# Performance work log

Measured on AMD Instinct MI355X. Metric: run time of the kernel, lower is better.

Reference implementation:

```python
import jax, jax.numpy as jnp
import numpy as np

N_HEADS = 8
EPS = 1e-12  # F.normalize eps


def setup_inputs() -> dict:
    key = jax.random.key(0)
    ks = jax.random.split(key, 7)
    B, M, S, D = 2, 4, 2048, 512
    scale = 1.0 / np.sqrt(D)
    return {
        "x": jax.random.normal(ks[0], (B, M, S, D), dtype=jnp.float32),
        "Wq": jax.random.normal(ks[1], (D, D), dtype=jnp.float32) * scale,
        "bq": jax.random.normal(ks[2], (D,), dtype=jnp.float32) * 0.01,
        "Wkv": jax.random.normal(ks[3], (D, D), dtype=jnp.float32) * scale,
        "bkv": jax.random.normal(ks[4], (D,), dtype=jnp.float32) * 0.01,
        "Wo": jax.random.normal(ks[5], (D, D), dtype=jnp.float32) * scale,
        "bo": jax.random.normal(ks[6], (D,), dtype=jnp.float32) * 0.01,
    }


def _heads(t, H):
    # [B,M,S,D] -> [B,M,H,S,dk]
    B, Mo, S, D = t.shape
    return t.reshape(B, Mo, S, H, D // H).swapaxes(2, 3)


def reference(x, Wq, bq, Wkv, bkv, Wo, bo):
    B, Mo, S, D = x.shape
    H = N_HEADS
    # nn.Linear: y = x @ W^T + b
    Q = x @ Wq.T + bq
    KV = x @ Wkv.T + bkv  # K and V share this projection
    Qh = _heads(Q, H)
    Kh = _heads(KV, H)
    Vh = Kh
    # L2-normalize along head dim (cosine attention)
    Qn = Qh / jnp.maximum(jnp.linalg.norm(Qh, axis=-1, keepdims=True), EPS)
    Kn = Kh / jnp.maximum(jnp.linalg.norm(Kh, axis=-1, keepdims=True), EPS)
    scores = jnp.einsum("bmhqd,bmhkd->bmhqk", Qn, Kn)
    attn = jax.nn.softmax(scores, axis=-1)  # dropout=0 (eval)
    ctx = jnp.einsum("bmhqk,bmhkd->bmhqd", attn, Vh)
    ctx = ctx.swapaxes(2, 3).reshape(B, Mo, S, D)
    return ctx @ Wo.T + bo
```

## Files before the change

### kernel.cpp

```cpp
#include <hip/hip_runtime.h>

typedef __attribute__((ext_vector_type(8))) short bf16x8;
typedef __attribute__((ext_vector_type(8))) _Float16 f16x8;
typedef __attribute__((ext_vector_type(2))) _Float16 f16x2;
typedef __attribute__((ext_vector_type(4))) float f32x4;
typedef __attribute__((ext_vector_type(16))) float f32x16;
typedef __attribute__((ext_vector_type(2))) unsigned int u32x2;

__device__ __forceinline__ unsigned short f2bf(float f) {
  union { float f; unsigned int i; } v;
  v.f = f;
  unsigned int r = v.i + 0x7FFFu + ((v.i >> 16) & 1u);
  return (unsigned short)(r >> 16);
}

__device__ __forceinline__ f16x2 cvt_pk(float a, float b) {
  return __builtin_bit_cast(f16x2, __builtin_amdgcn_cvt_pkrtz(a, b));
}

__device__ __forceinline__ unsigned as_u32(f16x2 x) {
  return __builtin_bit_cast(unsigned int, x);
}
__device__ __forceinline__ f16x2 as_f16x2(unsigned x) {
  return __builtin_bit_cast(f16x2, x);
}

#if __has_builtin(__builtin_amdgcn_permlane32_swap)
__device__ __forceinline__ u32x2 plswap(unsigned a, unsigned b) {
  return __builtin_amdgcn_permlane32_swap(a, b, false, false);
}
#else
__device__ __forceinline__ u32x2 plswap(unsigned a, unsigned b) {
  unsigned pa = (unsigned)__shfl_xor((int)a, 32);
  unsigned pb = (unsigned)__shfl_xor((int)b, 32);
  int hi = (int)(threadIdx.x & 32);
  u32x2 r;
  r.x = hi ? pb : a;
  r.y = hi ? b : pa;
  return r;
}
#endif

__device__ __forceinline__ f16x8 pack4(f16x2 a, f16x2 b, f16x2 c, f16x2 d) {
  union { f16x2 h[4]; f16x8 v; } u;
  u.h[0] = a; u.h[1] = b; u.h[2] = c; u.h[3] = d;
  return u.v;
}

__device__ __forceinline__ void gl_lds16(const unsigned short* g, unsigned short* l) {
  __builtin_amdgcn_global_load_lds(
      (const __attribute__((address_space(1))) unsigned int*)g,
      (__attribute__((address_space(3))) unsigned int*)l, 16, 0, 0);
}

__device__ __forceinline__ f16x2 exp_poly(f16x2 x) {
  const f16x2 a5 = {(_Float16)0.00868682f, (_Float16)0.00868682f};
  const f16x2 a4 = {(_Float16)0.04379392f, (_Float16)0.04379392f};
  const f16x2 a3 = {(_Float16)0.16648887f, (_Float16)0.16648887f};
  const f16x2 a2 = {(_Float16)0.49919676f, (_Float16)0.49919676f};
  const f16x2 a1 = {(_Float16)1.00002229f, (_Float16)1.00002229f};
  const f16x2 a0 = {(_Float16)1.00004478f, (_Float16)1.00004478f};
#if __has_builtin(__builtin_elementwise_fma)
  f16x2 r = a5;
  r = __builtin_elementwise_fma(r, x, a4);
  r = __builtin_elementwise_fma(r, x, a3);
  r = __builtin_elementwise_fma(r, x, a2);
  r = __builtin_elementwise_fma(r, x, a1);
  r = __builtin_elementwise_fma(r, x, a0);
#else
  f16x2 r = a5;
  r = r * x + a4;
  r = r * x + a3;
  r = r * x + a2;
  r = r * x + a1;
  r = r * x + a0;
#endif
  return r;
}

__device__ __forceinline__ float dot2acc(f16x2 a, float acc) {
#if __has_builtin(__builtin_amdgcn_fdot2)
  const f16x2 one2 = {(_Float16)1.0f, (_Float16)1.0f};
  return __builtin_amdgcn_fdot2(a, one2, acc, false);
#else
  return acc + (float)a.x + (float)a.y;
#endif
}

__global__ __launch_bounds__(256) void cvt_all(
    const float* __restrict__ x, const float* __restrict__ wq,
    const float* __restrict__ wkv, const float* __restrict__ wo,
    unsigned short* __restrict__ xf, unsigned short* __restrict__ wqf,
    unsigned short* __restrict__ wkvf, unsigned short* __restrict__ wof) {
  int b = blockIdx.x;
  const float* in;
  unsigned short* out;
  int i;
  if (b < 8192) { in = x; out = xf; i = b * 256 + threadIdx.x; }
  else if (b < 8448) { in = wq; out = wqf; i = (b - 8192) * 256 + threadIdx.x; }
  else if (b < 8704) { in = wkv; out = wkvf; i = (b - 8448) * 256 + threadIdx.x; }
  else { in = wo; out = wof; i = (b - 8704) * 256 + threadIdx.x; }
  float4 v = ((const float4*)in)[i];
  int f = i << 2;
  int row = f >> 9, c = f & 511;
  long off = ((((long)(row >> 7) * 8 + (c >> 6)) * 16 + ((row >> 4) & 7) * 2 +
               ((c >> 5) & 1)) * 64 + ((c >> 3) & 3) * 16 + (row & 15)) * 8 + (c & 7);
  ushort4 o;
  o.x = f2bf(v.x);
  o.y = f2bf(v.y);
  o.z = f2bf(v.z);
  o.w = f2bf(v.w);
  *(ushort4*)(out + off) = o;
}

__global__ __launch_bounds__(256) void gemm_qkv(
    const unsigned short* __restrict__ xf, const unsigned short* __restrict__ Wqf,
    const unsigned short* __restrict__ Wkvf, const float* __restrict__ bq,
    const float* __restrict__ bkv, unsigned short* __restrict__ Qn,
    unsigned short* __restrict__ Kf, unsigned short* __restrict__ Vf) {
  __shared__ __attribute__((aligned(16))) unsigned short lA[16 * 512];
  __shared__ __attribute__((aligned(16))) unsigned short lB[16 * 512];
  const int isKV = (int)(blockIdx.y >> 2);
  const unsigned short* Btf = isKV ? Wkvf : Wqf;
  const float* bias = isKV ? bkv : bq;
  const int tid = threadIdx.x;
  const int lane = tid & 63;
  const int quad = lane >> 4, m16 = lane & 15;
  const int w = tid >> 6;
  const int wm = w >> 1, wn = w & 1;
  const long mb = (long)blockIdx.x * 128;
  const int nt = (int)(blockIdx.y & 3);
  const long nb = (long)nt * 128;
  f32x4 acc[4][4];
#pragma unroll
  for (int i = 0; i < 4; i++)
#pragma unroll
    for (int j = 0; j < 4; j++) acc[i][j] = (f32x4){0.f, 0.f, 0.f, 0.f};

  for (int kb = 0; kb < 8; kb++) {
    __syncthreads();
    {
      const unsigned short* gA =
          xf + (((long)blockIdx.x * 8 + kb) * 16 + 4 * w) * 512 + lane * 8;
      gl_lds16(gA, &lA[(4 * w + 0) * 512]);
      gl_lds16(gA + 512, &lA[(4 * w + 1) * 512]);
      gl_lds16(gA + 1024, &lA[(4 * w + 2) * 512]);
      gl_lds16(gA + 1536, &lA[(4 * w + 3) * 512]);
      const unsigned short* gB =
          Btf + (((long)nt * 8 + kb) * 16 + 4 * w) * 512 + lane * 8;
      gl_lds16(gB, &lB[(4 * w + 0) * 512]);
      gl_lds16(gB + 512, &lB[(4 * w + 1) * 512]);
      gl_lds16(gB + 1024, &lB[(4 * w + 2) * 512]);
      gl_lds16(gB + 1536, &lB[(4 * w + 3) * 512]);
    }
    __syncthreads();
#pragma unroll
    for (int ks = 0; ks < 2; ks++) {
      bf16x8 af[4], bfr[4];
#pragma unroll
      for (int i = 0; i < 4; i++)
        af[i] = *(const bf16x8*)&lA[(((wm * 4 + i) << 1) | ks) * 512 + lane * 8];
#pragma unroll
      for (int j = 0; j < 4; j++)
        bfr[j] = *(const bf16x8*)&lB[(((wn * 4 + j) << 1) | ks) * 512 + lane * 8];
#pragma unroll
      for (int i = 0; i < 4; i++)
#pragma unroll
        for (int j = 0; j < 4; j++)
          acc[i][j] =
              __builtin_amdgcn_mfma_f32_16x16x32_bf16(af[i], bfr[j], acc[i][j], 0, 0, 0);
    }
  }
  const int h = (int)(nb >> 6) + wn;
#pragma unroll
  for (int i = 0; i < 4; i++) {
    long row0 = mb + wm * 64 + i * 16 + quad * 4;
    float bb[4], val[4][4], inv[4];
#pragma unroll
    for (int j = 0; j < 4; j++) {
      bb[j] = bias[nb + wn * 64 + j * 16 + m16];
#pragma unroll
      for (int r = 0; r < 4; r++) val[j][r] = acc[i][j][r] + bb[j];
    }
#pragma unroll
    for (int r = 0; r < 4; r++) {
      float s = val[0][r] * val[0][r] + val[1][r] * val[1][r] +
                val[2][r] * val[2][r] + val[3][r] * val[3][r];
      s += __shfl_xor(s, 1);
      s += __shfl_xor(s, 2);
      s += __shfl_xor(s, 4);
      s += __shfl_xor(s, 8);
      inv[r] = 1.0f / fmaxf(sqrtf(s), 1e-12f);
    }
    if (!isKV) {
#pragma unroll
      for (int r = 0; r < 4; r++)
#pragma unroll
        for (int j = 0; j < 4; j++) {
          long col = nb + wn * 64 + j * 16 + m16;
          Qn[(row0 + r) * 512 + col] = f2bf(val[j][r] * inv[r]);
        }
    } else {
      const int bm2 = (int)(row0 >> 11);
      const int gq = bm2 * 8 + h;
      const int kt = (int)((row0 & 2047) >> 6);
      const long tb = ((long)gq * 32 + kt) * 8;
#pragma unroll
      for (int j = 0; j < 4; j++) {
        long kb0 = (tb + (i >> 1) * 4 + j) * 512 +
                   ((((i & 1) * 16 + quad * 4) | ((m16 >> 3) << 5)) * 8) + (m16 & 7);
#pragma unroll
        for (int r = 0; r < 4; r++) Kf[kb0 + r * 8] = f2bf(val[j][r] * inv[r]);
      }
#pragma unroll
      for (int j = 0; j < 4; j++) {
        long vo = (tb + (j >> 1) * 4 + i) * 512 +
                  ((((j & 1) * 16 + m16) | ((quad >> 1) << 5)) * 8) + (quad & 1) * 4;
        f16x2 lo = cvt_pk(val[j][0], val[j][1]);
        f16x2 hi2 = cvt_pk(val[j][2], val[j][3]);
        uint2 pk = make_uint2(__builtin_bit_cast(unsigned int, lo),
                              __builtin_bit_cast(unsigned int, hi2));
        *(uint2*)(Vf + vo) = pk;
      }
    }
  }
}

__global__ __launch_bounds__(256) void gemm_o(
    const unsigned short* __restrict__ Af, const unsigned short* __restrict__ Btf,
    const float* __restrict__ bias, float* __restrict__ Cout) {
  __shared__ __attribute__((aligned(16))) unsigned short lA[16 * 512];
  __shared__ __attribute__((aligned(16))) unsigned short lB[16 * 512];
  const int tid = threadIdx.x;
  const int lane = tid & 63;
  const int quad = lane >> 4, m16 = lane & 15;
  const int w = tid >> 6;
  const int wm = w >> 1, wn = w & 1;
  const long mb = (long)blockIdx.x * 128;
  const int nt = (int)blockIdx.y;
  const long nb = (long)nt * 128;
  f32x4 acc[4][4];
#pragma unroll
  for (int i = 0; i < 4; i++)
#pragma unroll
    for (int j = 0; j < 4; j++) acc[i][j] = (f32x4){0.f, 0.f, 0.f, 0.f};

  for (int kb = 0; kb < 8; kb++) {
    __syncthreads();
    {
      const unsigned short* gA =
          Af + (((long)blockIdx.x * 8 + kb) * 16 + 4 * w) * 512 + lane * 8;
      gl_lds16(gA, &lA[(4 * w + 0) * 512]);
      gl_lds16(gA + 512, &lA[(4 * w + 1) * 512]);
      gl_lds16(gA + 1024, &lA[(4 * w + 2) * 512]);
      gl_lds16(gA + 1536, &lA[(4 * w + 3) * 512]);
      const unsigned short* gB =
          Btf + (((long)nt * 8 + kb) * 16 + 4 * w) * 512 + lane * 8;
      gl_lds16(gB, &lB[(4 * w + 0) * 512]);
      gl_lds16(gB + 512, &lB[(4 * w + 1) * 512]);
      gl_lds16(gB + 1024, &lB[(4 * w + 2) * 512]);
      gl_lds16(gB + 1536, &lB[(4 * w + 3) * 512]);
    }
    __syncthreads();
#pragma unroll
    for (int ks = 0; ks < 2; ks++) {
      bf16x8 af[4], bfr[4];
#pragma unroll
      for (int i = 0; i < 4; i++)
        af[i] = *(const bf16x8*)&lA[(((wm * 4 + i) << 1) | ks) * 512 + lane * 8];
#pragma unroll
      for (int j = 0; j < 4; j++)
        bfr[j] = *(const bf16x8*)&lB[(((wn * 4 + j) << 1) | ks) * 512 + lane * 8];
#pragma unroll
      for (int i = 0; i < 4; i++)
#pragma unroll
        for (int j = 0; j < 4; j++)
          acc[i][j] =
              __builtin_amdgcn_mfma_f32_16x16x32_bf16(af[i], bfr[j], acc[i][j], 0, 0, 0);
    }
  }
#pragma unroll
  for (int i = 0; i < 4; i++) {
    long row0 = mb + wm * 64 + i * 16 + quad * 4;
#pragma unroll
    for (int j = 0; j < 4; j++) {
      long col = nb + wn * 64 + j * 16 + m16;
      float bb = bias[col];
#pragma unroll
      for (int r = 0; r < 4; r++) Cout[(row0 + r) * 512 + col] = acc[i][j][r] + bb;
    }
  }
}

__global__ __launch_bounds__(512, 4) void attn_cos(
    const unsigned short* __restrict__ Qn, const unsigned short* __restrict__ Kf,
    const unsigned short* __restrict__ Vf, unsigned short* __restrict__ ctxf) {
  __shared__ __attribute__((aligned(16))) unsigned short lK[3][8 * 512];
  __shared__ __attribute__((aligned(16))) unsigned short lVt[3][8 * 512];
  const int id = (int)blockIdx.x;
  const int g = ((id >> 6) << 3) | (id & 7);
  const int qt = (id >> 3) & 7;
  const int bm = g >> 3, h = g & 7;
  const int tid = threadIdx.x;
  const int lane = tid & 63;
  const int l31 = lane & 31, hi = lane >> 5;
  const int w = tid >> 6;
  const long qrow0 = (long)bm * 2048 + qt * 256 + w * 32;
  const int colbase = h * 64;

  bf16x8 qf[4];
#pragma unroll
  for (int dd = 0; dd < 4; dd++)
    qf[dd] = *(const bf16x8*)(Qn + (qrow0 + l31) * 512 + colbase + dd * 16 + hi * 8);

  f32x16 cacc[2];
#pragma unroll
  for (int e = 0; e < 16; e++) { cacc[0][e] = 0.f; cacc[1][e] = 0.f; }
  float lacc = 0.f;

#define STAGE(buf, ktn)                                                  \
  {                                                                      \
    const long tb_ = ((long)g * 32 + (ktn)) * 8;                         \
    gl_lds16(Kf + (tb_ + w) * 512 + lane * 8, &lK[(buf)][w * 512]);      \
    gl_lds16(Vf + (tb_ + w) * 512 + lane * 8, &lVt[(buf)][w * 512]);     \
  }

  STAGE(0, 0);
  STAGE(1, 1);
  asm volatile("s_waitcnt vmcnt(2)" ::: "memory");
  __builtin_amdgcn_s_barrier();
  __builtin_amdgcn_sched_barrier(0);

  int cur = 0, nxt = 2;
  for (int kt = 0; kt < 32; ++kt) {
    STAGE(nxt, (kt + 2) & 31);
    __builtin_amdgcn_sched_barrier(0);
    const unsigned short* bK = lK[cur];
    const unsigned short* bV = lVt[cur];

    f32x16 sacc[2];
#pragma unroll
    for (int e = 0; e < 16; e++) { sacc[0][e] = 0.f; sacc[1][e] = 0.f; }
    __builtin_amdgcn_s_setprio(1);
#pragma unroll
    for (int dd = 0; dd < 4; dd++) {
      bf16x8 k0 = *(const bf16x8*)&bK[(0 * 4 + dd) * 512 + lane * 8];
      bf16x8 k1 = *(const bf16x8*)&bK[(1 * 4 + dd) * 512 + lane * 8];
      sacc[0] = __builtin_amdgcn_mfma_f32_32x32x16_bf16(k0, qf[dd], sacc[0], 0, 0, 0);
      sacc[1] = __builtin_amdgcn_mfma_f32_32x32x16_bf16(k1, qf[dd], sacc[1], 0, 0, 0);
    }
    __builtin_amdgcn_s_setprio(0);

    f16x2 pe[2][8];
#pragma unroll
    for (int kk = 0; kk < 2; kk++)
#pragma unroll
      for (int t = 0; t < 8; t++) {
        f16x2 x = cvt_pk(sacc[kk][2 * t], sacc[kk][2 * t + 1]);
        pe[kk][t] = exp_poly(x);
        lacc = dot2acc(pe[kk][t], lacc);
      }

    __builtin_amdgcn_s_setprio(1);
#pragma unroll
    for (int kk = 0; kk < 2; kk++)
#pragma unroll
      for (int s = 0; s < 2; s++) {
        u32x2 r0 = plswap(as_u32(pe[kk][4 * s + 0]), as_u32(pe[kk][4 * s + 2]));
        u32x2 r1 = plswap(as_u32(pe[kk][4 * s + 1]), as_u32(pe[kk][4 * s + 3]));
        f16x8 pa = pack4(as_f16x2(r0.x), as_f16x2(r1.x), as_f16x2(r0.y), as_f16x2(r1.y));
        const int ksub = kk * 2 + s;
        f16x8 v0 = *(const f16x8*)&bV[(0 * 4 + ksub) * 512 + lane * 8];
        f16x8 v1 = *(const f16x8*)&bV[(1 * 4 + ksub) * 512 + lane * 8];
        cacc[0] = __builtin_amdgcn_mfma_f32_32x32x16_f16(pa, v0, cacc[0], 0, 0, 0);
        cacc[1] = __builtin_amdgcn_mfma_f32_32x32x16_f16(pa, v1, cacc[1], 0, 0, 0);
      }
    __builtin_amdgcn_s_setprio(0);

    asm volatile("s_waitcnt vmcnt(2) lgkmcnt(0)" ::: "memory");
    __builtin_amdgcn_sched_barrier(0);
    __builtin_amdgcn_s_barrier();
    __builtin_amdgcn_sched_barrier(0);
    cur = (cur == 2) ? 0 : cur + 1;
    nxt = (nxt == 2) ? 0 : nxt + 1;
  }
#undef STAGE

  lacc += __shfl_xor(lacc, 32);
  float linv[16];
#pragma unroll
  for (int r = 0; r < 16; r++) {
    int qr = (r & 3) + 8 * (r >> 2) + 4 * hi;
    linv[r] = 1.0f / __shfl(lacc, qr);
  }

#pragma unroll
  for (int dt = 0; dt < 2; dt++) {
    const int c = colbase + dt * 32 + l31;
    const long ckb = (long)(c >> 6);
    const int cbit = (c >> 5) & 1;
    const int lane16 = ((c >> 3) & 3) * 16;
    const int e = c & 7;
#pragma unroll
    for (int r = 0; r < 16; r++) {
      long row = qrow0 + (r & 3) + 8 * (r >> 2) + 4 * hi;
      long off = ((((row >> 7) * 8 + ckb) * 16 + ((row >> 4) & 7) * 2 + cbit) * 64 +
                  lane16 + (row & 15)) * 8 + e;
      ctxf[off] = f2bf(cacc[dt][r] * linv[r]);
    }
  }
}

extern "C" void kernel_launch(void* const* d_in, const int* in_sizes, int n_in,
                              void* d_out, int out_size, void* d_ws, size_t ws_size,
                              hipStream_t stream) {
  (void)in_sizes; (void)n_in; (void)out_size; (void)ws_size;
  const float* x = (const float*)d_in[0];
  const float* Wq = (const float*)d_in[1];
  const float* bq = (const float*)d_in[2];
  const float* Wkv = (const float*)d_in[3];
  const float* bkv = (const float*)d_in[4];
  const float* Wo = (const float*)d_in[5];
  const float* bo = (const float*)d_in[6];

  char* ws = (char*)d_ws;
  unsigned short* xf     = (unsigned short*)(ws);
  unsigned short* Wqf    = (unsigned short*)(ws + 16777216);
  unsigned short* Wkvf   = (unsigned short*)(ws + 17301504);
  unsigned short* Wof    = (unsigned short*)(ws + 17825792);
  unsigned short* Qn_bf  = (unsigned short*)(ws + 18350080);
  unsigned short* Kf     = (unsigned short*)(ws + 35127296);
  unsigned short* Vf     = (unsigned short*)(ws + 51904512);
  unsigned short* ctxf   = xf;

  cvt_all<<<8960, 256, 0, stream>>>(x, Wq, Wkv, Wo, xf, Wqf, Wkvf, Wof);

  gemm_qkv<<<dim3(128, 8), 256, 0, stream>>>(xf, Wqf, Wkvf, bq, bkv, Qn_bf, Kf, Vf);

  attn_cos<<<512, 512, 0, stream>>>(Qn_bf, Kf, Vf, ctxf);

  gemm_o<<<dim3(128, 4), 256, 0, stream>>>(ctxf, Wof, bo, (float*)d_out);
}
```

Baseline: 230.3 us.

## Fuse fp32-to-bf16 conversion into GEMM loads and compute softmax sum via MFMA

Drops the separate cvt_all kernel. The QKV and output GEMMs now read fp32 x and weights directly and convert them to bf16 in registers before writing to LDS. This removes one launch plus a full write and re-read of the bf16 copy of x, but the GEMMs lose the async global-to-LDS path and issue more global traffic per tile. In attention, the per-lane fdot2 row-sum is replaced by an extra MFMA against a ones vector, which also removes the shuffles at the end, and the first score MFMA now starts from a zero constant instead of explicitly zeroed accumulators.

```diff
diff --git a/kernel.cpp b/kernel.cpp
--- a/kernel.cpp
+++ b/kernel.cpp
@@ -12,6 +12,12 @@
   v.f = f;
   unsigned int r = v.i + 0x7FFFu + ((v.i >> 16) & 1u);
   return (unsigned short)(r >> 16);
+}
+
+__device__ __forceinline__ unsigned cvt_pk_bf16(float a, float b) {
+  unsigned r;
+  asm("v_cvt_pk_bf16_f32 %0, %1, %2" : "=v"(r) : "v"(a), "v"(b));
+  return r;
 }
 
 __device__ __forceinline__ f16x2 cvt_pk(float a, float b) {
@@ -78,50 +84,15 @@
   return r;
 }
 
-__device__ __forceinline__ float dot2acc(f16x2 a, float acc) {
-#if __has_builtin(__builtin_amdgcn_fdot2)
-  const f16x2 one2 = {(_Float16)1.0f, (_Float16)1.0f};
-  return __builtin_amdgcn_fdot2(a, one2, acc, false);
-#else
-  return acc + (float)a.x + (float)a.y;
-#endif
-}
-
-__global__ __launch_bounds__(256) void cvt_all(
-    const float* __restrict__ x, const float* __restrict__ wq,
-    const float* __restrict__ wkv, const float* __restrict__ wo,
-    unsigned short* __restrict__ xf, unsigned short* __restrict__ wqf,
-    unsigned short* __restrict__ wkvf, unsigned short* __restrict__ wof) {
-  int b = blockIdx.x;
-  const float* in;
-  unsigned short* out;
-  int i;
-  if (b < 8192) { in = x; out = xf; i = b * 256 + threadIdx.x; }
-  else if (b < 8448) { in = wq; out = wqf; i = (b - 8192) * 256 + threadIdx.x; }
-  else if (b < 8704) { in = wkv; out = wkvf; i = (b - 8448) * 256 + threadIdx.x; }
-  else { in = wo; out = wof; i = (b - 8704) * 256 + threadIdx.x; }
-  float4 v = ((const float4*)in)[i];
-  int f = i << 2;
-  int row = f >> 9, c = f & 511;
-  long off = ((((long)(row >> 7) * 8 + (c >> 6)) * 16 + ((row >> 4) & 7) * 2 +
-               ((c >> 5) & 1)) * 64 + ((c >> 3) & 3) * 16 + (row & 15)) * 8 + (c & 7);
-  ushort4 o;
-  o.x = f2bf(v.x);
-  o.y = f2bf(v.y);
-  o.z = f2bf(v.z);
-  o.w = f2bf(v.w);
-  *(ushort4*)(out + off) = o;
-}
-
 __global__ __launch_bounds__(256) void gemm_qkv(
-    const unsigned short* __restrict__ xf, const unsigned short* __restrict__ Wqf,
-    const unsigned short* __restrict__ Wkvf, const float* __restrict__ bq,
+    const float* __restrict__ X, const float* __restrict__ Wq,
+    const float* __restrict__ Wkv, const float* __restrict__ bq,
     const float* __restrict__ bkv, unsigned short* __restrict__ Qn,
     unsigned short* __restrict__ Kf, unsigned short* __restrict__ Vf) {
   __shared__ __attribute__((aligned(16))) unsigned short lA[16 * 512];
   __shared__ __attribute__((aligned(16))) unsigned short lB[16 * 512];
   const int isKV = (int)(blockIdx.y >> 2);
-  const unsigned short* Btf = isKV ? Wkvf : Wqf;
+  const float* Wt = isKV ? Wkv : Wq;
   const float* bias = isKV ? bkv : bq;
   const int tid = threadIdx.x;
   const int lane = tid & 63;
@@ -140,18 +111,33 @@
   for (int kb = 0; kb < 8; kb++) {
     __syncthreads();
     {
-      const unsigned short* gA =
-          xf + (((long)blockIdx.x * 8 + kb) * 16 + 4 * w) * 512 + lane * 8;
-      gl_lds16(gA, &lA[(4 * w + 0) * 512]);
-      gl_lds16(gA + 512, &lA[(4 * w + 1) * 512]);
-      gl_lds16(gA + 1024, &lA[(4 * w + 2) * 512]);
-      gl_lds16(gA + 1536, &lA[(4 * w + 3) * 512]);
-      const unsigned short* gB =
-          Btf + (((long)nt * 8 + kb) * 16 + 4 * w) * 512 + lane * 8;
-      gl_lds16(gB, &lB[(4 * w + 0) * 512]);
-      gl_lds16(gB + 512, &lB[(4 * w + 1) * 512]);
-      gl_lds16(gB + 1024, &lB[(4 * w + 2) * 512]);
-      gl_lds16(gB + 1536, &lB[(4 * w + 3) * 512]);
+      float4 fa[4][2], fb[4][2];
+#pragma unroll
+      for (int t = 0; t < 4; t++) {
+        const int s = 4 * w + t;
+        const int col = kb * 64 + (s & 1) * 32 + quad * 8;
+        const float* pa = X + (mb + (s >> 1) * 16 + m16) * 512 + col;
+        fa[t][0] = *(const float4*)pa;
+        fa[t][1] = *(const float4*)(pa + 4);
+        const float* pb = Wt + (nb + (s >> 1) * 16 + m16) * 512 + col;
+        fb[t][0] = *(const float4*)pb;
+        fb[t][1] = *(const float4*)(pb + 4);
+      }
+#pragma unroll
+      for (int t = 0; t < 4; t++) {
+        const int s = 4 * w + t;
+        uint4 ca, cb;
+        ca.x = cvt_pk_bf16(fa[t][0].x, fa[t][0].y);
+        ca.y = cvt_pk_bf16(fa[t][0].z, fa[t][0].w);
+        ca.z = cvt_pk_bf16(fa[t][1].x, fa[t][1].y);
+        ca.w = cvt_pk_bf16(fa[t][1].z, fa[t][1].w);
+        *(uint4*)&lA[s * 512 + lane * 8] = ca;
+        cb.x = cvt_pk_bf16(fb[t][0].x, fb[t][0].y);
+        cb.y = cvt_pk_bf16(fb[t][0].z, fb[t][0].w);
+        cb.z = cvt_pk_bf16(fb[t][1].x, fb[t][1].y);
+        cb.w = cvt_pk_bf16(fb[t][1].z, fb[t][1].w);
+        *(uint4*)&lB[s * 512 + lane * 8] = cb;
+      }
     }
     __syncthreads();
 #pragma unroll
@@ -227,7 +213,7 @@
 }
 
 __global__ __launch_bounds__(256) void gemm_o(
-    const unsigned short* __restrict__ Af, const unsigned short* __restrict__ Btf,
+    const unsigned short* __restrict__ Af, const float* __restrict__ Wo,
     const float* __restrict__ bias, float* __restrict__ Cout) {
   __shared__ __attribute__((aligned(16))) unsigned short lA[16 * 512];
   __shared__ __attribute__((aligned(16))) unsigned short lB[16 * 512];
@@ -254,12 +240,25 @@
       gl_lds16(gA + 512, &lA[(4 * w + 1) * 512]);
       gl_lds16(gA + 1024, &lA[(4 * w + 2) * 512]);
       gl_lds16(gA + 1536, &lA[(4 * w + 3) * 512]);
-      const unsigned short* gB =
-          Btf + (((long)nt * 8 + kb) * 16 + 4 * w) * 512 + lane * 8;
-      gl_lds16(gB, &lB[(4 * w + 0) * 512]);
-      gl_lds16(gB + 512, &lB[(4 * w + 1) * 512]);
-      gl_lds16(gB + 1024, &lB[(4 * w + 2) * 512]);
-      gl_lds16(gB + 1536, &lB[(4 * w + 3) * 512]);
+      float4 fb[4][2];
+#pragma unroll
+      for (int t = 0; t < 4; t++) {
+        const int s = 4 * w + t;
+        const int col = kb * 64 + (s & 1) * 32 + quad * 8;
+        const float* pb = Wo + (nb + (s >> 1) * 16 + m16) * 512 + col;
+        fb[t][0] = *(const float4*)pb;
+        fb[t][1] = *(const float4*)(pb + 4);
+      }
+#pragma unroll
+      for (int t = 0; t < 4; t++) {
+        const int s = 4 * w + t;
+        uint4 cb;
+        cb.x = cvt_pk_bf16(fb[t][0].x, fb[t][0].y);
+        cb.y = cvt_pk_bf16(fb[t][0].z, fb[t][0].w);
+        cb.z = cvt_pk_bf16(fb[t][1].x, fb[t][1].y);
+        cb.w = cvt_pk_bf16(fb[t][1].z, fb[t][1].w);
+        *(uint4*)&lB[s * 512 + lane * 8] = cb;
+      }
     }
     __syncthreads();
 #pragma unroll
@@ -314,9 +313,12 @@
     qf[dd] = *(const bf16x8*)(Qn + (qrow0 + l31) * 512 + colbase + dd * 16 + hi * 8);
 
   f32x16 cacc[2];
-#pragma unroll
-  for (int e = 0; e < 16; e++) { cacc[0][e] = 0.f; cacc[1][e] = 0.f; }
-  float lacc = 0.f;
+  f32x16 caccl;
+#pragma unroll
+  for (int e = 0; e < 16; e++) { cacc[0][e] = 0.f; cacc[1][e] = 0.f; caccl[e] = 0.f; }
+  const f16x8 onesv = {(_Float16)1.0f, (_Float16)1.0f, (_Float16)1.0f, (_Float16)1.0f,
+                       (_Float16)1.0f, (_Float16)1.0f, (_Float16)1.0f, (_Float16)1.0f};
+  const f32x16 zv = {};
 
 #define STAGE(buf, ktn)                                                  \
   {                                                                      \
@@ -339,11 +341,15 @@
     const unsigned short* bV = lVt[cur];
 
     f32x16 sacc[2];
-#pragma unroll
-    for (int e = 0; e < 16; e++) { sacc[0][e] = 0.f; sacc[1][e] = 0.f; }
     __builtin_amdgcn_s_setprio(1);
-#pragma unroll
-    for (int dd = 0; dd < 4; dd++) {
+    {
+      bf16x8 k0 = *(const bf16x8*)&bK[(0 * 4 + 0) * 512 + lane * 8];
+      bf16x8 k1 = *(const bf16x8*)&bK[(1 * 4 + 0) * 512 + lane * 8];
+      sacc[0] = __builtin_amdgcn_mfma_f32_32x32x16_bf16(k0, qf[0], zv, 0, 0, 0);
+      sacc[1] = __builtin_amdgcn_mfma_f32_32x32x16_bf16(k1, qf[0], zv, 0, 0, 0);
+    }
+#pragma unroll
+    for (int dd = 1; dd < 4; dd++) {
       bf16x8 k0 = *(const bf16x8*)&bK[(0 * 4 + dd) * 512 + lane * 8];
       bf16x8 k1 = *(const bf16x8*)&bK[(1 * 4 + dd) * 512 + lane * 8];
       sacc[0] = __builtin_amdgcn_mfma_f32_32x32x16_bf16(k0, qf[dd], sacc[0], 0, 0, 0);
@@ -355,11 +361,8 @@
 #pragma unroll
     for (int kk = 0; kk < 2; kk++)
 #pragma unroll
-      for (int t = 0; t < 8; t++) {
-        f16x2 x = cvt_pk(sacc[kk][2 * t], sacc[kk][2 * t + 1]);
-        pe[kk][t] = exp_poly(x);
-        lacc = dot2acc(pe[kk][t], lacc);
-      }
+      for (int t = 0; t < 8; t++)
+        pe[kk][t] = exp_poly(cvt_pk(sacc[kk][2 * t], sacc[kk][2 * t + 1]));
 
     __builtin_amdgcn_s_setprio(1);
 #pragma unroll
@@ -374,6 +377,7 @@
         f16x8 v1 = *(const f16x8*)&bV[(1 * 4 + ksub) * 512 + lane * 8];
         cacc[0] = __builtin_amdgcn_mfma_f32_32x32x16_f16(pa, v0, cacc[0], 0, 0, 0);
         cacc[1] = __builtin_amdgcn_mfma_f32_32x32x16_f16(pa, v1, cacc[1], 0, 0, 0);
+        caccl = __builtin_amdgcn_mfma_f32_32x32x16_f16(pa, onesv, caccl, 0, 0, 0);
       }
     __builtin_amdgcn_s_setprio(0);
 
@@ -386,13 +390,9 @@
   }
 #undef STAGE
 
-  lacc += __shfl_xor(lacc, 32);
   float linv[16];
 #pragma unroll
-  for (int r = 0; r < 16; r++) {
-    int qr = (r & 3) + 8 * (r >> 2) + 4 * hi;
-    linv[r] = 1.0f / __shfl(lacc, qr);
-  }
+  for (int r = 0; r < 16; r++) linv[r] = 1.0f / caccl[r];
 
 #pragma unroll
   for (int dt = 0; dt < 2; dt++) {
@@ -424,20 +424,14 @@
   const float* bo = (const float*)d_in[6];
 
   char* ws = (char*)d_ws;
-  unsigned short* xf     = (unsigned short*)(ws);
-  unsigned short* Wqf    = (unsigned short*)(ws + 16777216);
-  unsigned short* Wkvf   = (unsigned short*)(ws + 17301504);
-  unsigned short* Wof    = (unsigned short*)(ws + 17825792);
-  unsigned short* Qn_bf  = (unsigned short*)(ws + 18350080);
-  unsigned short* Kf     = (unsigned short*)(ws + 35127296);
-  unsigned short* Vf     = (unsigned short*)(ws + 51904512);
-  unsigned short* ctxf   = xf;
-
-  cvt_all<<<8960, 256, 0, stream>>>(x, Wq, Wkv, Wo, xf, Wqf, Wkvf, Wof);
-
-  gemm_qkv<<<dim3(128, 8), 256, 0, stream>>>(xf, Wqf, Wkvf, bq, bkv, Qn_bf, Kf, Vf);
+  unsigned short* Qn_bf = (unsigned short*)(ws);
+  unsigned short* Kf    = (unsigned short*)(ws + 16777216);
+  unsigned short* Vf    = (unsigned short*)(ws + 33554432);
+  unsigned short* ctxf  = (unsigned short*)(ws + 50331648);
+
+  gemm_qkv<<<dim3(128, 8), 256, 0, stream>>>(x, Wq, Wkv, bq, bkv, Qn_bf, Kf, Vf);
 
   attn_cos<<<512, 512, 0, stream>>>(Qn_bf, Kf, Vf, ctxf);
 
-  gemm_o<<<dim3(128, 4), 256, 0, stream>>>(ctxf, Wof, bo, (float*)d_out);
-}
+  gemm_o<<<dim3(128, 4), 256, 0, stream>>>(ctxf, Wo, bo, (float*)d_out);
+}
```

New measurement: 267.1 us. +16.0%, slower.

## Stage QKV epilogue through LDS and compute softmax row sums via MFMA

Applied to the files above, without the earlier changes.

The QKV GEMM epilogue now writes normalized Q, K and V tiles into shared memory first, then copies them out with coalesced 16-byte global stores instead of scattered 2-byte stores. In attention, the softmax denominator is accumulated by an extra MFMA against a ones vector instead of per-lane dot2 adds and end-of-loop shuffles. The first QK MFMA also takes a zero accumulator directly, dropping the per-iteration zeroing. This adds syncthreads and LDS traffic in the epilogue, plus one extra MFMA per PV step in the inner loop.

```diff
diff --git a/kernel.cpp b/kernel.cpp
--- a/kernel.cpp
+++ b/kernel.cpp
@@ -76,15 +76,6 @@
   r = r * x + a0;
 #endif
   return r;
-}
-
-__device__ __forceinline__ float dot2acc(f16x2 a, float acc) {
-#if __has_builtin(__builtin_amdgcn_fdot2)
-  const f16x2 one2 = {(_Float16)1.0f, (_Float16)1.0f};
-  return __builtin_amdgcn_fdot2(a, one2, acc, false);
-#else
-  return acc + (float)a.x + (float)a.y;
-#endif
 }
 
 __global__ __launch_bounds__(256) void cvt_all(
@@ -118,8 +109,9 @@
     const unsigned short* __restrict__ Wkvf, const float* __restrict__ bq,
     const float* __restrict__ bkv, unsigned short* __restrict__ Qn,
     unsigned short* __restrict__ Kf, unsigned short* __restrict__ Vf) {
-  __shared__ __attribute__((aligned(16))) unsigned short lA[16 * 512];
-  __shared__ __attribute__((aligned(16))) unsigned short lB[16 * 512];
+  __shared__ __attribute__((aligned(16))) unsigned short smem[16384];
+  unsigned short* lA = smem;
+  unsigned short* lB = smem + 8192;
   const int isKV = (int)(blockIdx.y >> 2);
   const unsigned short* Btf = isKV ? Wkvf : Wqf;
   const float* bias = isKV ? bkv : bq;
@@ -171,56 +163,110 @@
               __builtin_amdgcn_mfma_f32_16x16x32_bf16(af[i], bfr[j], acc[i][j], 0, 0, 0);
     }
   }
-  const int h = (int)(nb >> 6) + wn;
-#pragma unroll
-  for (int i = 0; i < 4; i++) {
-    long row0 = mb + wm * 64 + i * 16 + quad * 4;
-    float bb[4], val[4][4], inv[4];
-#pragma unroll
-    for (int j = 0; j < 4; j++) {
-      bb[j] = bias[nb + wn * 64 + j * 16 + m16];
-#pragma unroll
-      for (int r = 0; r < 4; r++) val[j][r] = acc[i][j][r] + bb[j];
-    }
-#pragma unroll
-    for (int r = 0; r < 4; r++) {
-      float s = val[0][r] * val[0][r] + val[1][r] * val[1][r] +
-                val[2][r] * val[2][r] + val[3][r] * val[3][r];
-      s += __shfl_xor(s, 1);
-      s += __shfl_xor(s, 2);
-      s += __shfl_xor(s, 4);
-      s += __shfl_xor(s, 8);
-      inv[r] = 1.0f / fmaxf(sqrtf(s), 1e-12f);
-    }
-    if (!isKV) {
-#pragma unroll
-      for (int r = 0; r < 4; r++)
+
+  float bb[4], inv_s[4][4];
+#pragma unroll
+  for (int j = 0; j < 4; j++) bb[j] = bias[nb + wn * 64 + j * 16 + m16];
+  __syncthreads();
+
+  if (!isKV) {
+#pragma unroll
+    for (int i = 0; i < 4; i++) {
+      float val[4][4];
+#pragma unroll
+      for (int j = 0; j < 4; j++)
+#pragma unroll
+        for (int r = 0; r < 4; r++) val[j][r] = acc[i][j][r] + bb[j];
+#pragma unroll
+      for (int r = 0; r < 4; r++) {
+        float s = val[0][r] * val[0][r] + val[1][r] * val[1][r] +
+                  val[2][r] * val[2][r] + val[3][r] * val[3][r];
+        s += __shfl_xor(s, 1);
+        s += __shfl_xor(s, 2);
+        s += __shfl_xor(s, 4);
+        s += __shfl_xor(s, 8);
+        float inv = 1.0f / fmaxf(sqrtf(s), 1e-12f);
+#pragma unroll
+        for (int j = 0; j < 4; j++)
+          smem[(wm * 64 + i * 16 + quad * 4 + r) * 128 + wn * 64 + j * 16 + m16] =
+              f2bf(val[j][r] * inv);
+      }
+    }
+    __syncthreads();
+#pragma unroll
+    for (int it = 0; it < 8; it++) {
+      int row = w * 32 + it * 4 + (lane >> 4);
+      uint4 d = *(const uint4*)&smem[row * 128 + (lane & 15) * 8];
+      *(uint4*)&Qn[(mb + row) * 512 + nb + (lane & 15) * 8] = d;
+    }
+  } else {
+#pragma unroll
+    for (int i = 0; i < 4; i++) {
+      float val[4][4];
+#pragma unroll
+      for (int j = 0; j < 4; j++)
+#pragma unroll
+        for (int r = 0; r < 4; r++) val[j][r] = acc[i][j][r] + bb[j];
+#pragma unroll
+      for (int r = 0; r < 4; r++) {
+        float s = val[0][r] * val[0][r] + val[1][r] * val[1][r] +
+                  val[2][r] * val[2][r] + val[3][r] * val[3][r];
+        s += __shfl_xor(s, 1);
+        s += __shfl_xor(s, 2);
+        s += __shfl_xor(s, 4);
+        s += __shfl_xor(s, 8);
+        inv_s[i][r] = 1.0f / fmaxf(sqrtf(s), 1e-12f);
+      }
+      const int rb = (wn * 2 + wm) * 4096;
+#pragma unroll
+      for (int j = 0; j < 4; j++) {
+        const int slot = (i >> 1) * 4 + j;
+#pragma unroll
+        for (int r = 0; r < 4; r++) {
+          const int lf = (((i & 1) * 16 + quad * 4 + r) | ((m16 >> 3) << 5));
+          smem[rb + slot * 512 + lf * 8 + (m16 & 7)] = f2bf(val[j][r] * inv_s[i][r]);
+        }
+      }
+    }
+    __syncthreads();
+    {
+      const int hh = (int)(nb >> 6) + (w & 1);
+      const int gq = (int)(mb >> 11) * 8 + hh;
+      const int kt0 = (((int)(mb & 2047)) >> 6) + (w >> 1);
+      const long gb = ((long)gq * 32 + kt0) * 4096;
+      const int rb = ((w & 1) * 2 + (w >> 1)) * 4096;
+#pragma unroll
+      for (int it = 0; it < 8; it++) {
+        uint4 d = *(const uint4*)&smem[rb + it * 512 + lane * 8];
+        *(uint4*)&Kf[gb + it * 512 + lane * 8] = d;
+      }
+    }
+    __syncthreads();
+    {
+      const int rb = (wn * 2 + wm) * 4096;
+#pragma unroll
+      for (int i = 0; i < 4; i++)
 #pragma unroll
         for (int j = 0; j < 4; j++) {
-          long col = nb + wn * 64 + j * 16 + m16;
-          Qn[(row0 + r) * 512 + col] = f2bf(val[j][r] * inv[r]);
+          f16x2 lo = cvt_pk(acc[i][j][0] + bb[j], acc[i][j][1] + bb[j]);
+          f16x2 hi2 = cvt_pk(acc[i][j][2] + bb[j], acc[i][j][3] + bb[j]);
+          const int slot = (j >> 1) * 4 + i;
+          const int lf = (((j & 1) * 16 + m16) | ((quad >> 1) << 5));
+          *(uint2*)&smem[rb + slot * 512 + lf * 8 + (quad & 1) * 4] =
+              make_uint2(as_u32(lo), as_u32(hi2));
         }
-    } else {
-      const int bm2 = (int)(row0 >> 11);
-      const int gq = bm2 * 8 + h;
-      const int kt = (int)((row0 & 2047) >> 6);
-      const long tb = ((long)gq * 32 + kt) * 8;
-#pragma unroll
-      for (int j = 0; j < 4; j++) {
-        long kb0 = (tb + (i >> 1) * 4 + j) * 512 +
-                   ((((i & 1) * 16 + quad * 4) | ((m16 >> 3) << 5)) * 8) + (m16 & 7);
-#pragma unroll
-        for (int r = 0; r < 4; r++) Kf[kb0 + r * 8] = f2bf(val[j][r] * inv[r]);
-      }
-#pragma unroll
-      for (int j = 0; j < 4; j++) {
-        long vo = (tb + (j >> 1) * 4 + i) * 512 +
-                  ((((j & 1) * 16 + m16) | ((quad >> 1) << 5)) * 8) + (quad & 1) * 4;
-        f16x2 lo = cvt_pk(val[j][0], val[j][1]);
-        f16x2 hi2 = cvt_pk(val[j][2], val[j][3]);
-        uint2 pk = make_uint2(__builtin_bit_cast(unsigned int, lo),
-                              __builtin_bit_cast(unsigned int, hi2));
-        *(uint2*)(Vf + vo) = pk;
+    }
+    __syncthreads();
+    {
+      const int hh = (int)(nb >> 6) + (w & 1);
+      const int gq = (int)(mb >> 11) * 8 + hh;
+      const int kt0 = (((int)(mb & 2047)) >> 6) + (w >> 1);
+      const long gb = ((long)gq * 32 + kt0) * 4096;
+      const int rb = ((w & 1) * 2 + (w >> 1)) * 4096;
+#pragma unroll
+      for (int it = 0; it < 8; it++) {
+        uint4 d = *(const uint4*)&smem[rb + it * 512 + lane * 8];
+        *(uint4*)&Vf[gb + it * 512 + lane * 8] = d;
       }
     }
   }
@@ -314,9 +360,12 @@
     qf[dd] = *(const bf16x8*)(Qn + (qrow0 + l31) * 512 + colbase + dd * 16 + hi * 8);
 
   f32x16 cacc[2];
-#pragma unroll
-  for (int e = 0; e < 16; e++) { cacc[0][e] = 0.f; cacc[1][e] = 0.f; }
-  float lacc = 0.f;
+  f32x16 caccl;
+#pragma unroll
+  for (int e = 0; e < 16; e++) { cacc[0][e] = 0.f; cacc[1][e] = 0.f; caccl[e] = 0.f; }
+  const f16x8 onesv = {(_Float16)1.0f, (_Float16)1.0f, (_Float16)1.0f, (_Float16)1.0f,
+                       (_Float16)1.0f, (_Float16)1.0f, (_Float16)1.0f, (_Float16)1.0f};
+  const f32x16 zv = {};
 
 #define STAGE(buf, ktn)                                                  \
   {                                                                      \
@@ -339,11 +388,15 @@
     const unsigned short* bV = lVt[cur];
 
     f32x16 sacc[2];
-#pragma unroll
-    for (int e = 0; e < 16; e++) { sacc[0][e] = 0.f; sacc[1][e] = 0.f; }
     __builtin_amdgcn_s_setprio(1);
-#pragma unroll
-    for (int dd = 0; dd < 4; dd++) {
+    {
+      bf16x8 k0 = *(const bf16x8*)&bK[(0 * 4 + 0) * 512 + lane * 8];
+      bf16x8 k1 = *(const bf16x8*)&bK[(1 * 4 + 0) * 512 + lane * 8];
+      sacc[0] = __builtin_amdgcn_mfma_f32_32x32x16_bf16(k0, qf[0], zv, 0, 0, 0);
+      sacc[1] = __builtin_amdgcn_mfma_f32_32x32x16_bf16(k1, qf[0], zv, 0, 0, 0);
+    }
+#pragma unroll
+    for (int dd = 1; dd < 4; dd++) {
       bf16x8 k0 = *(const bf16x8*)&bK[(0 * 4 + dd) * 512 + lane * 8];
       bf16x8 k1 = *(const bf16x8*)&bK[(1 * 4 + dd) * 512 + lane * 8];
       sacc[0] = __builtin_amdgcn_mfma_f32_32x32x16_bf16(k0, qf[dd], sacc[0], 0, 0, 0);
@@ -355,11 +408,8 @@
 #pragma unroll
     for (int kk = 0; kk < 2; kk++)
 #pragma unroll
-      for (int t = 0; t < 8; t++) {
-        f16x2 x = cvt_pk(sacc[kk][2 * t], sacc[kk][2 * t + 1]);
-        pe[kk][t] = exp_poly(x);
-        lacc = dot2acc(pe[kk][t], lacc);
-      }
+      for (int t = 0; t < 8; t++)
+        pe[kk][t] = exp_poly(cvt_pk(sacc[kk][2 * t], sacc[kk][2 * t + 1]));
 
     __builtin_amdgcn_s_setprio(1);
 #pragma unroll
@@ -374,6 +424,7 @@
         f16x8 v1 = *(const f16x8*)&bV[(1 * 4 + ksub) * 512 + lane * 8];
         cacc[0] = __builtin_amdgcn_mfma_f32_32x32x16_f16(pa, v0, cacc[0], 0, 0, 0);
         cacc[1] = __builtin_amdgcn_mfma_f32_32x32x16_f16(pa, v1, cacc[1], 0, 0, 0);
+        caccl = __builtin_amdgcn_mfma_f32_32x32x16_f16(pa, onesv, caccl, 0, 0, 0);
       }
     __builtin_amdgcn_s_setprio(0);
 
@@ -386,13 +437,9 @@
   }
 #undef STAGE
 
-  lacc += __shfl_xor(lacc, 32);
   float linv[16];
 #pragma unroll
-  for (int r = 0; r < 16; r++) {
-    int qr = (r & 3) + 8 * (r >> 2) + 4 * hi;
-    linv[r] = 1.0f / __shfl(lacc, qr);
-  }
+  for (int r = 0; r < 16; r++) linv[r] = 1.0f / caccl[r];
 
 #pragma unroll
   for (int dt = 0; dt < 2; dt++) {
```

Measured after the change: 228.5 us. No clear change (-0.8%).
